# Optimization experiments

Measured on AMD Instinct MI355X. Metric: run time of the kernel, lower is better.

The kernel has to match this reference:

```python
import jax, jax.numpy as jnp
import numpy as np

B, S, D, H = 1, 4096, 512, 8
HD = D // H  # head_dims = 64


def setup_inputs() -> dict:
    key = jax.random.key(0)
    ks = jax.random.split(key, 12)
    scale = 0.02
    query = jax.random.normal(ks[0], (B, S, D), dtype=jnp.float32)
    key_t = jax.random.normal(ks[1], (B, S, D), dtype=jnp.float32)
    value = jax.random.normal(ks[2], (B, S, D), dtype=jnp.float32)
    mask = jax.random.randint(ks[3], (B, 1, S, S), 0, 2, dtype=jnp.int32)
    # per-head projection params (torch Linear: y = x @ W.T + b)
    Wq = jax.random.normal(ks[4], (HD, HD), dtype=jnp.float32) * scale
    bq = jax.random.normal(ks[5], (HD,), dtype=jnp.float32) * scale
    Wk = jax.random.normal(ks[6], (HD, HD), dtype=jnp.float32) * scale
    bk = jax.random.normal(ks[7], (HD,), dtype=jnp.float32) * scale
    Wv = jax.random.normal(ks[8], (HD, HD), dtype=jnp.float32) * scale
    bv = jax.random.normal(ks[9], (HD,), dtype=jnp.float32) * scale
    Wfc = jax.random.normal(ks[10], (D, D), dtype=jnp.float32) * scale
    bfc = jax.random.normal(ks[11], (D,), dtype=jnp.float32) * scale
    return {"query": query, "key": key_t, "value": value, "mask": mask,
            "Wq": Wq, "bq": bq, "Wk": Wk, "bk": bk, "Wv": Wv, "bv": bv,
            "Wfc": Wfc, "bfc": bfc}


def reference(query, key, value, mask, Wq, bq, Wk, bk, Wv, bv, Wfc, bfc):
    Batch, q_len, _ = query.shape
    k_len = key.shape[1]
    # reshape to [b, s, h, d] then apply per-head linear projections
    q = query.reshape(Batch, q_len, H, HD) @ Wq.T + bq
    k = key.reshape(Batch, k_len, H, HD) @ Wk.T + bk
    v = value.reshape(Batch, k_len, H, HD) @ Wv.T + bv
    # raw scores [b, h, q, k]; mask applied BEFORE scaling (as in original)
    score = jnp.einsum('bqhd,bkhd->bhqk', q, k)
    score = jnp.where(mask == 0, jnp.float32(-1e20), score)
    attn = jax.nn.softmax(score / jnp.sqrt(jnp.float32(HD)), axis=-1)
    out = jnp.einsum('bhqv,bvhd->bqhd', attn, v).reshape(Batch, q_len, D)
    return out @ Wfc.T + bfc
```

## Files before the change

### kernel.cpp

```cpp
#include <hip/hip_runtime.h>
#include <hip/hip_bf16.h>

#define S_LEN 4096
#define DMODEL 512
#define NHEAD 8
#define HDIM 64

typedef __bf16 bf16x8 __attribute__((ext_vector_type(8)));
typedef __bf16 bf16x4 __attribute__((ext_vector_type(4)));
typedef float f32x4 __attribute__((ext_vector_type(4)));

#define S2EXP 0.18033688011112042f

__device__ __forceinline__ void gload_lds16(const void* g, void* l) {
    __builtin_amdgcn_global_load_lds((const __attribute__((address_space(1))) void*)g,
                                     (__attribute__((address_space(3))) void*)l, 16, 0, 0);
}

__global__ __launch_bounds__(256) void proj_all_kernel(const float* __restrict__ xq,
                                                       const float* __restrict__ xk,
                                                       const float* __restrict__ xv,
                                                       const float* __restrict__ Wq,
                                                       const float* __restrict__ bq,
                                                       const float* __restrict__ Wk,
                                                       const float* __restrict__ bk,
                                                       const float* __restrict__ Wv,
                                                       const float* __restrict__ bv,
                                                       __bf16* __restrict__ yq,
                                                       __bf16* __restrict__ yk,
                                                       __bf16* __restrict__ vt) {
    __shared__ float T[64][65];
    int bid = blockIdx.x;
    int t = threadIdx.x, wave = t >> 6, lane = t & 63, lg = lane >> 4, lc = lane & 15;
    if (bid < 512) {
        int r0 = bid * 64 + wave * 16;
        const float* xrq = xq + (size_t)(r0 + lc) * 64 + lg * 8;
        const float* xrk = xk + (size_t)(r0 + lc) * 64 + lg * 8;
        bf16x8 aq[2], ak[2];
#pragma unroll
        for (int c = 0; c < 2; ++c) {
            f32x4 u0 = *(const f32x4*)(xrq + c * 32);
            f32x4 u1 = *(const f32x4*)(xrq + c * 32 + 4);
            f32x4 v0 = *(const f32x4*)(xrk + c * 32);
            f32x4 v1 = *(const f32x4*)(xrk + c * 32 + 4);
            bf16x8 a, b;
#pragma unroll
            for (int j = 0; j < 4; ++j) {
                a[j] = (__bf16)u0[j]; a[4 + j] = (__bf16)u1[j];
                b[j] = (__bf16)v0[j]; b[4 + j] = (__bf16)v1[j];
            }
            aq[c] = a; ak[c] = b;
        }
#pragma unroll
        for (int nt = 0; nt < 4; ++nt) {
            const float* wq = Wq + (size_t)(nt * 16 + lc) * 64 + lg * 8;
            const float* wk = Wk + (size_t)(nt * 16 + lc) * 64 + lg * 8;
            f32x4 cq = {0, 0, 0, 0}, ck = {0, 0, 0, 0};
#pragma unroll
            for (int c = 0; c < 2; ++c) {
                f32x4 u0 = *(const f32x4*)(wq + c * 32);
                f32x4 u1 = *(const f32x4*)(wq + c * 32 + 4);
                f32x4 v0 = *(const f32x4*)(wk + c * 32);
                f32x4 v1 = *(const f32x4*)(wk + c * 32 + 4);
                bf16x8 bw, bw2;
#pragma unroll
                for (int j = 0; j < 4; ++j) {
                    bw[j] = (__bf16)u0[j]; bw[4 + j] = (__bf16)u1[j];
                    bw2[j] = (__bf16)v0[j]; bw2[4 + j] = (__bf16)v1[j];
                }
                cq = __builtin_amdgcn_mfma_f32_16x16x32_bf16(aq[c], bw, cq, 0, 0, 0);
                ck = __builtin_amdgcn_mfma_f32_16x16x32_bf16(ak[c], bw2, ck, 0, 0, 0);
            }
            float bqv = bq[nt * 16 + lc], bkv = bk[nt * 16 + lc];
#pragma unroll
            for (int r = 0; r < 4; ++r) {
                yq[(size_t)(r0 + lg * 4 + r) * 64 + nt * 16 + lc] = (__bf16)(cq[r] + bqv);
                yk[(size_t)(r0 + lg * 4 + r) * 64 + nt * 16 + lc] = (__bf16)(ck[r] + bkv);
            }
        }
    } else {
        int vb = bid - 512;
        int h = vb & 7, s0 = (vb >> 3) * 64;
        const float* xr = xv + ((size_t)(s0 + wave * 16 + lc) * 8 + h) * 64 + lg * 8;
        bf16x8 av[2];
#pragma unroll
        for (int c = 0; c < 2; ++c) {
            f32x4 u0 = *(const f32x4*)(xr + c * 32);
            f32x4 u1 = *(const f32x4*)(xr + c * 32 + 4);
            bf16x8 a;
#pragma unroll
            for (int j = 0; j < 4; ++j) { a[j] = (__bf16)u0[j]; a[4 + j] = (__bf16)u1[j]; }
            av[c] = a;
        }
#pragma unroll
        for (int nt = 0; nt < 4; ++nt) {
            const float* wv = Wv + (size_t)(nt * 16 + lc) * 64 + lg * 8;
            f32x4 cv = {0, 0, 0, 0};
#pragma unroll
            for (int c = 0; c < 2; ++c) {
                f32x4 u0 = *(const f32x4*)(wv + c * 32);
                f32x4 u1 = *(const f32x4*)(wv + c * 32 + 4);
                bf16x8 bw;
#pragma unroll
                for (int j = 0; j < 4; ++j) { bw[j] = (__bf16)u0[j]; bw[4 + j] = (__bf16)u1[j]; }
                cv = __builtin_amdgcn_mfma_f32_16x16x32_bf16(av[c], bw, cv, 0, 0, 0);
            }
            float bvv = bv[nt * 16 + lc];
#pragma unroll
            for (int r = 0; r < 4; ++r) T[wave * 16 + lg * 4 + r][nt * 16 + lc] = cv[r] + bvv;
        }
        __syncthreads();
        int d = t >> 2, qr = t & 3;
        bf16x8 w0, w1;
#pragma unroll
        for (int i = 0; i < 8; ++i) {
            w0[i] = (__bf16)T[qr * 16 + i][d];
            w1[i] = (__bf16)T[qr * 16 + 8 + i][d];
        }
        __bf16* dst = vt + ((size_t)h * 64 + d) * 4096 + s0 + qr * 16;
        *(bf16x8*)(dst) = w0;
        *(bf16x8*)(dst + 8) = w1;
    }
}

__global__ __launch_bounds__(256) void prep_kernel(const int* __restrict__ mask,
                                                   unsigned int* __restrict__ pack,
                                                   const float* __restrict__ Wfc,
                                                   __bf16* __restrict__ wfc_bf) {
    int bid = blockIdx.x;
    int t = threadIdx.x;
    if (bid < 2048) {
        int lane = t & 63;
        int wid = bid * 4 + (t >> 6);
#pragma unroll 4
        for (int it = 0; it < 32; ++it) {
            int gw = wid * 32 + it;
            int qi = gw >> 6, seg = gw & 63;
            unsigned long long bits = __ballot(mask[(size_t)qi * 4096 + seg * 64 + lane] != 0);
            if (lane == 0)
                *(unsigned long long*)(&pack[(size_t)qi * 128 + seg * 2]) = bits;
        }
    } else {
        int b = bid - 2048;
        const f32x4* s4 = (const f32x4*)Wfc;
#pragma unroll
        for (int i = 0; i < 8; ++i) {
            int idx = (b * 8 + i) * 256 + t;
            f32x4 v = s4[idx];
            bf16x4 o;
#pragma unroll
            for (int j = 0; j < 4; ++j) o[j] = (__bf16)v[j];
            *(bf16x4*)(wfc_bf + (size_t)idx * 4) = o;
        }
    }
}

__global__ __launch_bounds__(256, 4) void attn_kernel(const __bf16* __restrict__ qb,
                                                      const __bf16* __restrict__ kb,
                                                      const __bf16* __restrict__ vt,
                                                      const unsigned int* __restrict__ mp,
                                                      int kv_len,
                                                      float* __restrict__ opart,
                                                      float* __restrict__ stats,
                                                      __bf16* __restrict__ ao) {
    int bid = blockIdx.x;
    int h = bid & 7, qt = (bid >> 3) & 63, sp = bid >> 9;
    int kv0 = sp * kv_len;
    int t = threadIdx.x, wave = t >> 6, lane = t & 63, lg = lane >> 4, lc = lane & 15;
    int q0 = qt * 64 + wave * 16;

    __shared__ __bf16 Kt[2][64 * 64];
    __shared__ __bf16 Vt[2][64 * 64];
    __shared__ __bf16 P[4][16 * 64];

    int srow = lane >> 3;
    int cg = (lane & 7) ^ srow;

    const __bf16* qrow = qb + ((size_t)(q0 + lc) * 8 + h) * 64 + lg * 8;
    bf16x8 qf0 = *(const bf16x8*)(qrow);
    bf16x8 qf1 = *(const bf16x8*)(qrow + 32);

    bf16x8 onesf;
#pragma unroll
    for (int j = 0; j < 8; ++j) onesf[j] = (__bf16)1.0f;

    f32x4 o0 = {0,0,0,0}, o1 = {0,0,0,0}, o2 = {0,0,0,0}, o3 = {0,0,0,0};
    f32x4 l_acc = {0,0,0,0};

    const unsigned int* mrow = mp + (size_t)(q0 + lc) * 128;
    const __bf16* vbase = vt + (size_t)h * 64 * 4096;

#pragma unroll
    for (int j = wave * 2; j < wave * 2 + 2; ++j) {
        gload_lds16(kb + (size_t)(kv0 + j * 8 + srow) * 512 + h * 64 + cg * 8, &Kt[0][j * 512]);
        gload_lds16(vbase + (size_t)(j * 8 + srow) * 4096 + kv0 + cg * 8,      &Vt[0][j * 512]);
    }
    __syncthreads();

    int nsteps = kv_len >> 6;
    for (int step = 0; step < nsteps; ++step) {
        int cur = step & 1;
        int kb_i = kv0 + step * 64;
        if (step < nsteps - 1) {
            int nxt = kb_i + 64;
#pragma unroll
            for (int j = wave * 2; j < wave * 2 + 2; ++j) {
                gload_lds16(kb + (size_t)(nxt + j * 8 + srow) * 512 + h * 64 + cg * 8, &Kt[cur ^ 1][j * 512]);
                gload_lds16(vbase + (size_t)(j * 8 + srow) * 4096 + nxt + cg * 8,      &Vt[cur ^ 1][j * 512]);
            }
        }
        const char* Kb = (const char*)&Kt[cur][0];
        f32x4 sc[4];
#pragma unroll
        for (int kc = 0; kc < 4; ++kc) {
            int row = kc * 16 + lc;
            int sw = (row & 7) << 4;
            bf16x8 kf0 = *(const bf16x8*)(Kb + ((row * 128 + lg * 16) ^ sw));
            bf16x8 kf1 = *(const bf16x8*)(Kb + ((row * 128 + 64 + lg * 16) ^ sw));
            f32x4 z = {0,0,0,0};
            z = __builtin_amdgcn_mfma_f32_16x16x32_bf16(kf0, qf0, z, 0, 0, 0);
            z = __builtin_amdgcn_mfma_f32_16x16x32_bf16(kf1, qf1, z, 0, 0, 0);
            sc[kc] = z;
        }
        uint2 mw = *(const uint2*)(mrow + (kb_i >> 5));
        char* pbase = (char*)&P[wave][0];
#pragma unroll
        for (int kc = 0; kc < 4; ++kc) {
            unsigned int wsel = (kc < 2) ? mw.x : mw.y;
            bf16x4 pk;
#pragma unroll
            for (int r = 0; r < 4; ++r) {
                int bitpos = (kc & 1) * 16 + lg * 4 + r;
                float p = __builtin_amdgcn_exp2f(sc[kc][r] * S2EXP);
                int sel = ((int)(wsel << (31 - bitpos))) >> 31;
                pk[r] = (__bf16)__int_as_float(__float_as_int(p) & sel);
            }
            int byte = (lc * 128 + kc * 32 + lg * 8) ^ ((lc & 7) << 4);
            *(bf16x4*)(pbase + byte) = pk;
        }
        const char* Vb = (const char*)&Vt[cur][0];
        int swv = (lc & 7) << 4;
#pragma unroll
        for (int kk = 0; kk < 2; ++kk) {
            int pbyte = (lc * 128 + kk * 64 + lg * 16) ^ swv;
            bf16x8 pf = *(const bf16x8*)((const char*)&P[wave][0] + pbyte);
            l_acc = __builtin_amdgcn_mfma_f32_16x16x32_bf16(pf, onesf, l_acc, 0, 0, 0);
            int ch = (kk * 4 + lg) * 16;
            o0 = __builtin_amdgcn_mfma_f32_16x16x32_bf16(pf, *(const bf16x8*)(Vb + (((0 * 16 + lc) * 128 + ch) ^ swv)), o0, 0, 0, 0);
            o1 = __builtin_amdgcn_mfma_f32_16x16x32_bf16(pf, *(const bf16x8*)(Vb + (((1 * 16 + lc) * 128 + ch) ^ swv)), o1, 0, 0, 0);
            o2 = __builtin_amdgcn_mfma_f32_16x16x32_bf16(pf, *(const bf16x8*)(Vb + (((2 * 16 + lc) * 128 + ch) ^ swv)), o2, 0, 0, 0);
            o3 = __builtin_amdgcn_mfma_f32_16x16x32_bf16(pf, *(const bf16x8*)(Vb + (((3 * 16 + lc) * 128 + ch) ^ swv)), o3, 0, 0, 0);
        }
        __syncthreads();
    }
    if (opart) {
        if (lc == 0) {
#pragma unroll
            for (int r = 0; r < 4; ++r)
                stats[(size_t)sp * 32768 + (size_t)(q0 + lg * 4 + r) * 8 + h] = l_acc[r];
        }
#pragma unroll
        for (int r = 0; r < 4; ++r) {
            size_t rh = (size_t)sp * 32768 + (size_t)(q0 + lg * 4 + r) * 8 + h;
            float* dst = opart + rh * 64;
            dst[0 * 16 + lc] = o0[r];
            dst[1 * 16 + lc] = o1[r];
            dst[2 * 16 + lc] = o2[r];
            dst[3 * 16 + lc] = o3[r];
        }
    } else {
#pragma unroll
        for (int r = 0; r < 4; ++r) {
            float inv = 1.0f / l_acc[r];
            int row = q0 + lg * 4 + r;
            __bf16* dst = ao + (size_t)row * 512 + h * 64;
            dst[0 * 16 + lc] = (__bf16)(o0[r] * inv);
            dst[1 * 16 + lc] = (__bf16)(o1[r] * inv);
            dst[2 * 16 + lc] = (__bf16)(o2[r] * inv);
            dst[3 * 16 + lc] = (__bf16)(o3[r] * inv);
        }
    }
}

__global__ __launch_bounds__(256) void combine_kernel(const float* __restrict__ opart,
                                                      const float* __restrict__ stats,
                                                      __bf16* __restrict__ ao) {
    int t = threadIdx.x, lane = t & 63, w = t >> 6;
    int rh = blockIdx.x * 4 + w;
    float L = stats[rh] + stats[32768 + rh];
    float acc = opart[(size_t)rh * 64 + lane] + opart[(size_t)(32768 + rh) * 64 + lane];
    int row = rh >> 3, h = rh & 7;
    ao[(size_t)row * 512 + h * 64 + lane] = (__bf16)(acc / L);
}

__global__ __launch_bounds__(256) void fc_kernel(const __bf16* __restrict__ ao,
                                                 const __bf16* __restrict__ Wb,
                                                 const float* __restrict__ bfc,
                                                 float* __restrict__ out) {
    int bid = blockIdx.x;
    int stile = bid >> 3, nt = bid & 7;
    int t = threadIdx.x, wave = t >> 6, lane = t & 63, lg = lane >> 4, lc = lane & 15;
    int s0 = stile * 64 + wave * 16;
    int n0 = nt * 64;
    f32x4 c0 = {0,0,0,0}, c1 = {0,0,0,0}, c2 = {0,0,0,0}, c3 = {0,0,0,0};
    for (int k0 = 0; k0 < 512; k0 += 32) {
        bf16x8 af = *(const bf16x8*)(ao + (size_t)(s0 + lc) * 512 + k0 + lg * 8);
        const __bf16* wb = Wb + k0 + lg * 8;
        c0 = __builtin_amdgcn_mfma_f32_16x16x32_bf16(af, *(const bf16x8*)(wb + (size_t)(n0 + 0 * 16 + lc) * 512), c0, 0, 0, 0);
        c1 = __builtin_amdgcn_mfma_f32_16x16x32_bf16(af, *(const bf16x8*)(wb + (size_t)(n0 + 1 * 16 + lc) * 512), c1, 0, 0, 0);
        c2 = __builtin_amdgcn_mfma_f32_16x16x32_bf16(af, *(const bf16x8*)(wb + (size_t)(n0 + 2 * 16 + lc) * 512), c2, 0, 0, 0);
        c3 = __builtin_amdgcn_mfma_f32_16x16x32_bf16(af, *(const bf16x8*)(wb + (size_t)(n0 + 3 * 16 + lc) * 512), c3, 0, 0, 0);
    }
#pragma unroll
    for (int r = 0; r < 4; ++r) {
        int row = s0 + lg * 4 + r;
        float* dst = out + (size_t)row * 512 + n0;
        dst[0 * 16 + lc] = c0[r] + bfc[n0 + 0 * 16 + lc];
        dst[1 * 16 + lc] = c1[r] + bfc[n0 + 1 * 16 + lc];
        dst[2 * 16 + lc] = c2[r] + bfc[n0 + 2 * 16 + lc];
        dst[3 * 16 + lc] = c3[r] + bfc[n0 + 3 * 16 + lc];
    }
}

extern "C" void kernel_launch(void* const* d_in, const int* in_sizes, int n_in,
                              void* d_out, int out_size, void* d_ws, size_t ws_size,
                              hipStream_t stream) {
    const float* query = (const float*)d_in[0];
    const float* key   = (const float*)d_in[1];
    const float* value = (const float*)d_in[2];
    const int*   mask  = (const int*)d_in[3];
    const float* Wq  = (const float*)d_in[4];
    const float* bq  = (const float*)d_in[5];
    const float* Wk  = (const float*)d_in[6];
    const float* bk  = (const float*)d_in[7];
    const float* Wv  = (const float*)d_in[8];
    const float* bv  = (const float*)d_in[9];
    const float* Wfc = (const float*)d_in[10];
    const float* bfc = (const float*)d_in[11];

    char* ws = (char*)d_ws;
    const size_t MB = 1024 * 1024;
    __bf16* q_bf   = (__bf16*)(ws + 0 * MB);
    __bf16* k_bf   = (__bf16*)(ws + 4 * MB);
    __bf16* vt     = (__bf16*)(ws + 8 * MB);
    __bf16* ao     = (__bf16*)(ws + 12 * MB);
    __bf16* wfc_bf = (__bf16*)(ws + 16 * MB);
    unsigned int* mpack = (unsigned int*)(ws + 17 * MB);
    const size_t base = 19 * MB;
    int nsplit = (ws_size >= base + 2 * (8 * MB) + 524288) ? 2 : 1;
    float* opart = (float*)(ws + base);
    float* stats = (float*)(ws + base + (size_t)nsplit * 8 * MB);

    proj_all_kernel<<<1024, 256, 0, stream>>>(query, key, value, Wq, bq, Wk, bk, Wv, bv,
                                              q_bf, k_bf, vt);
    prep_kernel<<<2080, 256, 0, stream>>>(mask, mpack, Wfc, wfc_bf);
    if (nsplit > 1) {
        attn_kernel<<<512 * nsplit, 256, 0, stream>>>(q_bf, k_bf, vt, mpack,
                                                      S_LEN / nsplit, opart, stats, ao);
        combine_kernel<<<8192, 256, 0, stream>>>(opart, stats, ao);
    } else {
        attn_kernel<<<512, 256, 0, stream>>>(q_bf, k_bf, vt, mpack,
                                             S_LEN, nullptr, nullptr, ao);
    }
    fc_kernel<<<512, 256, 0, stream>>>(ao, wfc_bf, bfc, (float*)d_out);
}
```

Measured before the change: 124.2 us.

## Fuse pre-kernels, halve attention KV tile for occupancy, allow 4-way KV split

Merges the projection and mask/weight prep kernels into a single launch to cut launch overhead. The attention kernel now processes 32-key tiles instead of 64, shrinking LDS and register use with new swizzle patterns so up to 8 blocks can reside per CU. The split-KV factor can rise to 4 when the workspace allows, and the combine kernel sums a variable number of partials. Smaller tiles add more barriers and loop overhead per key, and more splits add partial-output traffic.

```diff
diff --git a/kernel.cpp b/kernel.cpp
--- a/kernel.cpp
+++ b/kernel.cpp
@@ -17,18 +17,22 @@
                                      (__attribute__((address_space(3))) void*)l, 16, 0, 0);
 }
 
-__global__ __launch_bounds__(256) void proj_all_kernel(const float* __restrict__ xq,
-                                                       const float* __restrict__ xk,
-                                                       const float* __restrict__ xv,
-                                                       const float* __restrict__ Wq,
-                                                       const float* __restrict__ bq,
-                                                       const float* __restrict__ Wk,
-                                                       const float* __restrict__ bk,
-                                                       const float* __restrict__ Wv,
-                                                       const float* __restrict__ bv,
-                                                       __bf16* __restrict__ yq,
-                                                       __bf16* __restrict__ yk,
-                                                       __bf16* __restrict__ vt) {
+__global__ __launch_bounds__(256) void pre_kernel(const float* __restrict__ xq,
+                                                  const float* __restrict__ xk,
+                                                  const float* __restrict__ xv,
+                                                  const float* __restrict__ Wq,
+                                                  const float* __restrict__ bq,
+                                                  const float* __restrict__ Wk,
+                                                  const float* __restrict__ bk,
+                                                  const float* __restrict__ Wv,
+                                                  const float* __restrict__ bv,
+                                                  __bf16* __restrict__ yq,
+                                                  __bf16* __restrict__ yk,
+                                                  __bf16* __restrict__ vt,
+                                                  const int* __restrict__ mask,
+                                                  unsigned int* __restrict__ pack,
+                                                  const float* __restrict__ Wfc,
+                                                  __bf16* __restrict__ wfc_bf) {
     __shared__ float T[64][65];
     int bid = blockIdx.x;
     int t = threadIdx.x, wave = t >> 6, lane = t & 63, lg = lane >> 4, lc = lane & 15;
@@ -78,7 +82,7 @@
                 yk[(size_t)(r0 + lg * 4 + r) * 64 + nt * 16 + lc] = (__bf16)(ck[r] + bkv);
             }
         }
-    } else {
+    } else if (bid < 1024) {
         int vb = bid - 512;
         int h = vb & 7, s0 = (vb >> 3) * 64;
         const float* xr = xv + ((size_t)(s0 + wave * 16 + lc) * 8 + h) * 64 + lg * 8;
@@ -120,18 +124,8 @@
         __bf16* dst = vt + ((size_t)h * 64 + d) * 4096 + s0 + qr * 16;
         *(bf16x8*)(dst) = w0;
         *(bf16x8*)(dst + 8) = w1;
-    }
-}
-
-__global__ __launch_bounds__(256) void prep_kernel(const int* __restrict__ mask,
-                                                   unsigned int* __restrict__ pack,
-                                                   const float* __restrict__ Wfc,
-                                                   __bf16* __restrict__ wfc_bf) {
-    int bid = blockIdx.x;
-    int t = threadIdx.x;
-    if (bid < 2048) {
-        int lane = t & 63;
-        int wid = bid * 4 + (t >> 6);
+    } else if (bid < 3072) {
+        int wid = (bid - 1024) * 4 + (t >> 6);
 #pragma unroll 4
         for (int it = 0; it < 32; ++it) {
             int gw = wid * 32 + it;
@@ -141,7 +135,7 @@
                 *(unsigned long long*)(&pack[(size_t)qi * 128 + seg * 2]) = bits;
         }
     } else {
-        int b = bid - 2048;
+        int b = bid - 3072;
         const f32x4* s4 = (const f32x4*)Wfc;
 #pragma unroll
         for (int i = 0; i < 8; ++i) {
@@ -155,7 +149,7 @@
     }
 }
 
-__global__ __launch_bounds__(256, 4) void attn_kernel(const __bf16* __restrict__ qb,
+__global__ __launch_bounds__(256, 8) void attn_kernel(const __bf16* __restrict__ qb,
                                                       const __bf16* __restrict__ kb,
                                                       const __bf16* __restrict__ vt,
                                                       const unsigned int* __restrict__ mp,
@@ -169,12 +163,14 @@
     int t = threadIdx.x, wave = t >> 6, lane = t & 63, lg = lane >> 4, lc = lane & 15;
     int q0 = qt * 64 + wave * 16;
 
-    __shared__ __bf16 Kt[2][64 * 64];
-    __shared__ __bf16 Vt[2][64 * 64];
-    __shared__ __bf16 P[4][16 * 64];
-
-    int srow = lane >> 3;
-    int cg = (lane & 7) ^ srow;
+    __shared__ __bf16 Kt[2][32 * 64];
+    __shared__ __bf16 Vt[2][64 * 32];
+    __shared__ __bf16 P[4][16 * 32];
+
+    int srK = lane >> 3;
+    int cgK = (lane & 7) ^ srK;
+    int srV = lane >> 2;
+    int cgV = (lane & 3) ^ (srV & 3);
 
     const __bf16* qrow = qb + ((size_t)(q0 + lc) * 8 + h) * 64 + lg * 8;
     bf16x8 qf0 = *(const bf16x8*)(qrow);
@@ -190,29 +186,23 @@
     const unsigned int* mrow = mp + (size_t)(q0 + lc) * 128;
     const __bf16* vbase = vt + (size_t)h * 64 * 4096;
 
-#pragma unroll
-    for (int j = wave * 2; j < wave * 2 + 2; ++j) {
-        gload_lds16(kb + (size_t)(kv0 + j * 8 + srow) * 512 + h * 64 + cg * 8, &Kt[0][j * 512]);
-        gload_lds16(vbase + (size_t)(j * 8 + srow) * 4096 + kv0 + cg * 8,      &Vt[0][j * 512]);
-    }
+    gload_lds16(kb + (size_t)(kv0 + wave * 8 + srK) * 512 + h * 64 + cgK * 8, &Kt[0][wave * 512]);
+    gload_lds16(vbase + (size_t)(wave * 16 + srV) * 4096 + kv0 + cgV * 8,     &Vt[0][wave * 512]);
     __syncthreads();
 
-    int nsteps = kv_len >> 6;
+    int nsteps = kv_len >> 5;
     for (int step = 0; step < nsteps; ++step) {
         int cur = step & 1;
-        int kb_i = kv0 + step * 64;
+        int kb_i = kv0 + step * 32;
         if (step < nsteps - 1) {
-            int nxt = kb_i + 64;
-#pragma unroll
-            for (int j = wave * 2; j < wave * 2 + 2; ++j) {
-                gload_lds16(kb + (size_t)(nxt + j * 8 + srow) * 512 + h * 64 + cg * 8, &Kt[cur ^ 1][j * 512]);
-                gload_lds16(vbase + (size_t)(j * 8 + srow) * 4096 + nxt + cg * 8,      &Vt[cur ^ 1][j * 512]);
-            }
+            int nxt = kb_i + 32;
+            gload_lds16(kb + (size_t)(nxt + wave * 8 + srK) * 512 + h * 64 + cgK * 8, &Kt[cur ^ 1][wave * 512]);
+            gload_lds16(vbase + (size_t)(wave * 16 + srV) * 4096 + nxt + cgV * 8,     &Vt[cur ^ 1][wave * 512]);
         }
         const char* Kb = (const char*)&Kt[cur][0];
-        f32x4 sc[4];
-#pragma unroll
-        for (int kc = 0; kc < 4; ++kc) {
+        f32x4 sc[2];
+#pragma unroll
+        for (int kc = 0; kc < 2; ++kc) {
             int row = kc * 16 + lc;
             int sw = (row & 7) << 4;
             bf16x8 kf0 = *(const bf16x8*)(Kb + ((row * 128 + lg * 16) ^ sw));
@@ -222,34 +212,33 @@
             z = __builtin_amdgcn_mfma_f32_16x16x32_bf16(kf1, qf1, z, 0, 0, 0);
             sc[kc] = z;
         }
-        uint2 mw = *(const uint2*)(mrow + (kb_i >> 5));
+        unsigned int mw = mrow[kb_i >> 5];
         char* pbase = (char*)&P[wave][0];
-#pragma unroll
-        for (int kc = 0; kc < 4; ++kc) {
-            unsigned int wsel = (kc < 2) ? mw.x : mw.y;
+        int psw = (lc & 3) << 4;
+#pragma unroll
+        for (int kc = 0; kc < 2; ++kc) {
             bf16x4 pk;
 #pragma unroll
             for (int r = 0; r < 4; ++r) {
-                int bitpos = (kc & 1) * 16 + lg * 4 + r;
+                int bitpos = kc * 16 + lg * 4 + r;
                 float p = __builtin_amdgcn_exp2f(sc[kc][r] * S2EXP);
-                int sel = ((int)(wsel << (31 - bitpos))) >> 31;
+                int sel = ((int)(mw << (31 - bitpos))) >> 31;
                 pk[r] = (__bf16)__int_as_float(__float_as_int(p) & sel);
             }
-            int byte = (lc * 128 + kc * 32 + lg * 8) ^ ((lc & 7) << 4);
+            int byte = (lc * 64 + kc * 32 + lg * 8) ^ psw;
             *(bf16x4*)(pbase + byte) = pk;
         }
         const char* Vb = (const char*)&Vt[cur][0];
-        int swv = (lc & 7) << 4;
-#pragma unroll
-        for (int kk = 0; kk < 2; ++kk) {
-            int pbyte = (lc * 128 + kk * 64 + lg * 16) ^ swv;
-            bf16x8 pf = *(const bf16x8*)((const char*)&P[wave][0] + pbyte);
-            l_acc = __builtin_amdgcn_mfma_f32_16x16x32_bf16(pf, onesf, l_acc, 0, 0, 0);
-            int ch = (kk * 4 + lg) * 16;
-            o0 = __builtin_amdgcn_mfma_f32_16x16x32_bf16(pf, *(const bf16x8*)(Vb + (((0 * 16 + lc) * 128 + ch) ^ swv)), o0, 0, 0, 0);
-            o1 = __builtin_amdgcn_mfma_f32_16x16x32_bf16(pf, *(const bf16x8*)(Vb + (((1 * 16 + lc) * 128 + ch) ^ swv)), o1, 0, 0, 0);
-            o2 = __builtin_amdgcn_mfma_f32_16x16x32_bf16(pf, *(const bf16x8*)(Vb + (((2 * 16 + lc) * 128 + ch) ^ swv)), o2, 0, 0, 0);
-            o3 = __builtin_amdgcn_mfma_f32_16x16x32_bf16(pf, *(const bf16x8*)(Vb + (((3 * 16 + lc) * 128 + ch) ^ swv)), o3, 0, 0, 0);
+        bf16x8 pf = *(const bf16x8*)(pbase + ((lc * 64 + lg * 16) ^ psw));
+        l_acc = __builtin_amdgcn_mfma_f32_16x16x32_bf16(pf, onesf, l_acc, 0, 0, 0);
+#pragma unroll
+        for (int dt = 0; dt < 4; ++dt) {
+            int row = dt * 16 + lc;
+            bf16x8 vf = *(const bf16x8*)(Vb + ((row * 64 + lg * 16) ^ ((row & 3) << 4)));
+            if (dt == 0) o0 = __builtin_amdgcn_mfma_f32_16x16x32_bf16(pf, vf, o0, 0, 0, 0);
+            if (dt == 1) o1 = __builtin_amdgcn_mfma_f32_16x16x32_bf16(pf, vf, o1, 0, 0, 0);
+            if (dt == 2) o2 = __builtin_amdgcn_mfma_f32_16x16x32_bf16(pf, vf, o2, 0, 0, 0);
+            if (dt == 3) o3 = __builtin_amdgcn_mfma_f32_16x16x32_bf16(pf, vf, o3, 0, 0, 0);
         }
         __syncthreads();
     }
@@ -284,11 +273,15 @@
 
 __global__ __launch_bounds__(256) void combine_kernel(const float* __restrict__ opart,
                                                       const float* __restrict__ stats,
-                                                      __bf16* __restrict__ ao) {
+                                                      __bf16* __restrict__ ao, int nsplit) {
     int t = threadIdx.x, lane = t & 63, w = t >> 6;
     int rh = blockIdx.x * 4 + w;
-    float L = stats[rh] + stats[32768 + rh];
-    float acc = opart[(size_t)rh * 64 + lane] + opart[(size_t)(32768 + rh) * 64 + lane];
+    float L = 0.f, acc = 0.f;
+#pragma unroll 4
+    for (int sp = 0; sp < nsplit; ++sp) {
+        L += stats[(size_t)sp * 32768 + rh];
+        acc += opart[((size_t)sp * 32768 + rh) * 64 + lane];
+    }
     int row = rh >> 3, h = rh & 7;
     ao[(size_t)row * 512 + h * 64 + lane] = (__bf16)(acc / L);
 }
@@ -347,17 +340,18 @@
     __bf16* wfc_bf = (__bf16*)(ws + 16 * MB);
     unsigned int* mpack = (unsigned int*)(ws + 17 * MB);
     const size_t base = 19 * MB;
-    int nsplit = (ws_size >= base + 2 * (8 * MB) + 524288) ? 2 : 1;
+    int nsplit = 1;
+    if (ws_size >= base + 4 * (8 * MB) + 4 * 131072) nsplit = 4;
+    else if (ws_size >= base + 2 * (8 * MB) + 2 * 131072) nsplit = 2;
     float* opart = (float*)(ws + base);
     float* stats = (float*)(ws + base + (size_t)nsplit * 8 * MB);
 
-    proj_all_kernel<<<1024, 256, 0, stream>>>(query, key, value, Wq, bq, Wk, bk, Wv, bv,
-                                              q_bf, k_bf, vt);
-    prep_kernel<<<2080, 256, 0, stream>>>(mask, mpack, Wfc, wfc_bf);
+    pre_kernel<<<3104, 256, 0, stream>>>(query, key, value, Wq, bq, Wk, bk, Wv, bv,
+                                         q_bf, k_bf, vt, mask, mpack, Wfc, wfc_bf);
     if (nsplit > 1) {
         attn_kernel<<<512 * nsplit, 256, 0, stream>>>(q_bf, k_bf, vt, mpack,
                                                       S_LEN / nsplit, opart, stats, ao);
-        combine_kernel<<<8192, 256, 0, stream>>>(opart, stats, ao);
+        combine_kernel<<<8192, 256, 0, stream>>>(opart, stats, ao, nsplit);
     } else {
         attn_kernel<<<512, 256, 0, stream>>>(q_bf, k_bf, vt, mpack,
                                              S_LEN, nullptr, nullptr, ao);
```

Result: slower. 221.8 us (+78.6%).
